# Optimization experiments

Hardware: AMD Instinct MI355X
Metric: run time of the kernel (lower is better)

## Reference

```python
import jax, jax.numpy as jnp
import numpy as np

N = 100000
E = 1600000


def gcn_conv(x, src, dst, W, b, n_nodes):
    # PyG GCNConv: h = x @ W; symmetric norm with self-loops; scatter-add to dst; + bias
    h = x @ W
    deg = jnp.ones((n_nodes,), h.dtype).at[dst].add(jnp.ones((src.shape[0],), h.dtype))  # deg includes self-loop
    dis = jax.lax.rsqrt(deg)  # deg >= 1 so safe
    norm = dis[src] * dis[dst]  # [E]
    agg = jax.ops.segment_sum(norm[:, None] * h[src], dst, num_segments=n_nodes)
    agg = agg + (dis * dis)[:, None] * h  # self-loop contribution (norm = 1/deg_i)
    return agg + b


def setup_inputs() -> dict:
    key = jax.random.key(0)
    ks = jax.random.split(key, 10)
    x = jax.random.normal(ks[0], (N, 500), dtype=jnp.float32)
    edge_index = jax.random.randint(ks[1], (2, E), 0, N, dtype=jnp.int64)
    def glorot(k, fan_in, fan_out):
        s = jnp.sqrt(6.0 / (fan_in + fan_out))
        return jax.random.uniform(k, (fan_in, fan_out), jnp.float32, -s, s)
    return {
        "x": x,
        "edge_index": edge_index,
        "W0": glorot(ks[2], 500, 128), "b0": jnp.zeros((128,), jnp.float32),
        "W1": glorot(ks[3], 128, 128), "b1": jnp.zeros((128,), jnp.float32),
        "W2": glorot(ks[4], 128, 128), "b2": jnp.zeros((128,), jnp.float32),
        "Wfc": glorot(ks[5], 128, 40), "bfc": jnp.zeros((40,), jnp.float32),
    }


def reference(x, edge_index, W0, b0, W1, b1, W2, b2, Wfc, bfc):
    src, dst = edge_index[0], edge_index[1]
    # eval mode: dropout(p=0.2, training=False) is identity
    h = jax.nn.relu(gcn_conv(x, src, dst, W0, b0, N))
    h = jax.nn.relu(gcn_conv(h, src, dst, W1, b1, N))
    h = jax.nn.relu(gcn_conv(h, src, dst, W2, b2, N))
    logits = h @ Wfc + bfc
    return jax.nn.log_softmax(logits, axis=1)
```

## Files before the change

### kernel.cpp

```cpp
#include <hip/hip_runtime.h>
#include <hip/hip_bf16.h>
#include <cstdint>
#include <cstddef>

#define FIN 500
#define FH  128
#define FOUT 40
#define NB 256

typedef __attribute__((ext_vector_type(8))) short short8;
typedef __attribute__((ext_vector_type(4))) float f32x4;

__device__ inline float bf_lo(unsigned v) { unsigned t = v << 16; return __builtin_bit_cast(float, t); }
__device__ inline float bf_hi(unsigned v) { unsigned t = v & 0xffff0000u; return __builtin_bit_cast(float, t); }
__device__ inline unsigned short f2bf_bits(float f) {
  __hip_bfloat16 b = __float2bfloat16(f);
  return __builtin_bit_cast(unsigned short, b);
}


__global__ void __launch_bounds__(256) k_bcount(const int* __restrict__ dst,
                                                int* __restrict__ bucketCnt, int E) {
  __shared__ int lc[NB];
  int t = threadIdx.x;
  lc[t] = 0;
  __syncthreads();
  int base = blockIdx.x * 2048 + t * 8;
#pragma unroll
  for (int j = 0; j < 8; ++j) {
    int e = base + j;
    if (e < E) atomicAdd(&lc[dst[e] >> 9], 1);
  }
  __syncthreads();
  if (lc[t]) atomicAdd(&bucketCnt[t], lc[t]);
}

__global__ void k_bscan(const int* __restrict__ bucketCnt, int* __restrict__ bucketBase) {
  __shared__ int s[NB];
  int t = threadIdx.x;
  int v = bucketCnt[t];
  s[t] = v;
  __syncthreads();
  for (int o = 1; o < NB; o <<= 1) {
    int u = 0;
    if (t >= o) u = s[t - o];
    __syncthreads();
    if (t >= o) s[t] += u;
    __syncthreads();
  }
  bucketBase[t] = s[t] - v;
  if (t == NB - 1) bucketBase[NB] = s[NB - 1];
}

__global__ void __launch_bounds__(256) k_bin(const int* __restrict__ src,
                                             const int* __restrict__ dst,
                                             const int* __restrict__ bucketBase,
                                             int* __restrict__ bucketFill,
                                             int2* __restrict__ ebin, int E) {
  __shared__ int lc[NB];
  __shared__ int lbb[NB];
  int t = threadIdx.x;
  lc[t] = 0;
  lbb[t] = bucketBase[t];
  __syncthreads();
  int base = blockIdx.x * 2048 + t * 8;
  int rk[8], bk[8], dd[8], ss[8];
#pragma unroll
  for (int j = 0; j < 8; ++j) {
    int e = base + j;
    if (e < E) {
      dd[j] = dst[e]; ss[j] = src[e];
      bk[j] = dd[j] >> 9;
      rk[j] = atomicAdd(&lc[bk[j]], 1);
    }
  }
  __syncthreads();
  int c = lc[t];
  int gb = 0;
  if (c) gb = atomicAdd(&bucketFill[t], c);
  __syncthreads();
  lc[t] = gb;
  __syncthreads();
#pragma unroll
  for (int j = 0; j < 8; ++j) {
    int e = base + j;
    if (e < E) {
      int pos = lbb[bk[j]] + lc[bk[j]] + rk[j];
      ebin[pos] = make_int2(ss[j], dd[j]);
    }
  }
}

__global__ void __launch_bounds__(512) k_bhist(const int2* __restrict__ ebin,
                                               const int* __restrict__ bucketBase,
                                               int* __restrict__ cnt, int N) {
  __shared__ int hc[512];
  int t = threadIdx.x, b = blockIdx.x;
  hc[t] = 0;
  __syncthreads();
  int s = bucketBase[b], e = bucketBase[b + 1];
  for (int i = s + t; i < e; i += 512) atomicAdd(&hc[ebin[i].y & 511], 1);
  __syncthreads();
  int idx = b * 512 + t;
  if (idx < N) cnt[idx] = hc[t];
}

__global__ void __launch_bounds__(512) k_fscatter(const int2* __restrict__ ebin,
                                                  const int* __restrict__ bucketBase,
                                                  const int* __restrict__ rp,
                                                  const float* __restrict__ dis,
                                                  int2* __restrict__ epackS, int N) {
  __shared__ int lrp[512];
  __shared__ float ldis[512];
  __shared__ int fill[512];
  int t = threadIdx.x, b = blockIdx.x;
  int n0 = b * 512 + t;
  lrp[t] = (n0 < N) ? rp[n0] : 0;
  ldis[t] = (n0 < N) ? dis[n0] : 0.f;
  fill[t] = 0;
  __syncthreads();
  int s = bucketBase[b], e = bucketBase[b + 1];
  for (int i = s + t; i < e; i += 512) {
    int2 ed = ebin[i];
    int ld = ed.y & 511;
    int r = atomicAdd(&fill[ld], 1);
    float nm = dis[ed.x] * ldis[ld];
    epackS[lrp[ld] + r] = make_int2(ed.x << 7, __builtin_bit_cast(int, nm));
  }
}


__global__ void k_dis(const int* __restrict__ cnt, float* __restrict__ dis, int n) {
  int i = blockIdx.x * 256 + threadIdx.x;
  if (i < n) dis[i] = rsqrtf((float)cnt[i] + 1.0f);
}

__global__ void k_scan1(const int* __restrict__ cnt, int* __restrict__ rp,
                        int* __restrict__ bsums, int n) {
  __shared__ int sums[256];
  int t = threadIdx.x;
  int base = blockIdx.x * 1024;
  int c[4]; int tot = 0;
#pragma unroll
  for (int j = 0; j < 4; ++j) {
    int idx = base + t * 4 + j;
    c[j] = (idx < n) ? cnt[idx] : 0;
    tot += c[j];
  }
  sums[t] = tot;
  __syncthreads();
  for (int off = 1; off < 256; off <<= 1) {
    int v = 0;
    if (t >= off) v = sums[t - off];
    __syncthreads();
    if (t >= off) sums[t] += v;
    __syncthreads();
  }
  int run = sums[t] - tot;
#pragma unroll
  for (int j = 0; j < 4; ++j) {
    int idx = base + t * 4 + j;
    if (idx < n) rp[idx] = run;
    run += c[j];
  }
  if (t == 255) bsums[blockIdx.x] = sums[255];
}

__global__ void k_scan2(int* __restrict__ bsums, int nb) {
  __shared__ int s[256];
  int t = threadIdx.x;
  int v = (t < nb) ? bsums[t] : 0;
  s[t] = v;
  __syncthreads();
  for (int off = 1; off < 256; off <<= 1) {
    int u = 0;
    if (t >= off) u = s[t - off];
    __syncthreads();
    if (t >= off) s[t] += u;
    __syncthreads();
  }
  if (t < nb) bsums[t] = s[t] - v;
}

__global__ void k_scan3(int* __restrict__ rp, const int* __restrict__ bsums, int n, int E) {
  int idx = blockIdx.x * 256 + threadIdx.x;
  if (idx < n) rp[idx] += bsums[idx >> 10];
  if (idx == n) rp[n] = E;
}

__global__ void k_rescale(const int2* __restrict__ epackS, const float* __restrict__ scale,
                          int2* __restrict__ epackL, int E) {
  int e = blockIdx.x * 256 + threadIdx.x;
  if (e >= E) return;
  int2 p = epackS[e];
  float n = __builtin_bit_cast(float, p.y) * scale[p.x >> 7];
  epackL[e] = make_int2(p.x, __builtin_bit_cast(int, n));
}


__global__ void k_prep_w(const float* __restrict__ W, short* __restrict__ WT, int K, int KPAD) {
  int idx = blockIdx.x * 256 + threadIdx.x;
  if (idx >= 128 * KPAD) return;
  int c = idx / KPAD, k = idx - c * KPAD;
  WT[idx] = (k < K) ? (short)f2bf_bits(W[(size_t)k * FH + c]) : (short)0;
}

__global__ void k_prep_wfc(const float* __restrict__ Wfc, short* __restrict__ WfcT) {
  int idx = blockIdx.x * 256 + threadIdx.x;
  if (idx >= 48 * 128) return;
  int c = idx >> 7, k = idx & 127;
  WfcT[idx] = (c < FOUT) ? (short)f2bf_bits(Wfc[(size_t)k * FOUT + c]) : (short)0;
}


template<int KP, bool AF32>
__global__ void __launch_bounds__(512) k_gemm_q(const void* __restrict__ Aptr,
                                                const short* __restrict__ WT,
                                                unsigned char* __restrict__ hQ,
                                                float* __restrict__ scale,
                                                int M, int K) {
  constexpr int KPB = KP * 2;
  constexpr int NKT = KP / 32;
  __shared__ char sB[128 * KPB];
  __shared__ unsigned char lq[8][16 * 128];
  const int tid = threadIdx.x;
  const int wave = tid >> 6, lane = tid & 63;
  const int lr = lane & 15, g = lane >> 4;
  const int swz = (lr & 7) << 4;

  for (int idx = tid; idx < 16 * KP; idx += 512) {
    int c = idx / (KP / 8);
    int kq = idx - c * (KP / 8);
    short8 v = *(const short8*)(WT + (size_t)c * KP + kq * 8);
    *(short8*)(sB + (size_t)c * KPB + ((kq * 16) ^ ((c & 7) << 4))) = v;
  }
  __syncthreads();

  const int nStrips = M >> 4;
  for (int sid = blockIdx.x * 8 + wave; sid < nStrips; sid += gridDim.x * 8) {
    const int rowbase = sid * 16;
    const int arow = rowbase + lr;

    f32x4 acc[8];
#pragma unroll
    for (int j = 0; j < 8; ++j) acc[j] = (f32x4){0.f, 0.f, 0.f, 0.f};

    auto loadA = [&](int kt, short8& dstv) {
      const int k0 = kt * 32 + g * 8;
      if constexpr (AF32) {
        const float* A = (const float*)Aptr + (size_t)arow * K;
        float f[8];
        if (k0 + 8 <= K) {
          float4 u0 = *(const float4*)(A + k0);
          float4 u1 = *(const float4*)(A + k0 + 4);
          f[0] = u0.x; f[1] = u0.y; f[2] = u0.z; f[3] = u0.w;
          f[4] = u1.x; f[5] = u1.y; f[6] = u1.z; f[7] = u1.w;
        } else {
#pragma unroll
          for (int j = 0; j < 8; ++j) f[j] = (k0 + j < K) ? A[k0 + j] : 0.f;
        }
#pragma unroll
        for (int j = 0; j < 8; ++j) dstv[j] = (short)f2bf_bits(f[j]);
      } else {
        dstv = *(const short8*)((const short*)Aptr + (size_t)arow * K + k0);
      }
    };

    short8 aC, aN;
    loadA(0, aC);
#pragma unroll
    for (int kt = 0; kt < NKT; ++kt) {
      if (kt + 1 < NKT) loadA(kt + 1, aN);
      const int kofs = (kt * 64 + g * 16) ^ swz;
#pragma unroll
      for (int j = 0; j < 8; ++j) {
        short8 b = *(const short8*)(sB + (size_t)(j * 16 + lr) * KPB + kofs);
        acc[j] = __builtin_amdgcn_mfma_f32_16x16x32_bf16(aC, b, acc[j], 0, 0, 0);
      }
      aC = aN;
    }

    float mx[4];
#pragma unroll
    for (int r = 0; r < 4; ++r) {
      float m = 0.f;
#pragma unroll
      for (int j = 0; j < 8; ++j) m = fmaxf(m, fabsf(acc[j][r]));
#pragma unroll
      for (int s = 1; s < 16; s <<= 1) m = fmaxf(m, __shfl_xor(m, s));
      mx[r] = m;
    }
    if (lr == 0) {
      float4 sv = make_float4(mx[0] * (1.f / 127.f), mx[1] * (1.f / 127.f),
                              mx[2] * (1.f / 127.f), mx[3] * (1.f / 127.f));
      *(float4*)(scale + rowbase + g * 4) = sv;
    }
    float rs[4];
#pragma unroll
    for (int r = 0; r < 4; ++r) rs[r] = (mx[r] > 0.f) ? 127.f / mx[r] : 0.f;
#pragma unroll
    for (int j = 0; j < 8; ++j) {
#pragma unroll
      for (int r = 0; r < 4; ++r) {
        int q = (int)rintf(acc[j][r] * rs[r]);
        lq[wave][(g * 4 + r) * 128 + j * 16 + lr] = (unsigned char)(signed char)q;
      }
    }
    asm volatile("s_waitcnt lgkmcnt(0)" ::: "memory");
    __builtin_amdgcn_sched_barrier(0);
    {
      int o = lane * 32;
      *(uint4*)(hQ + (size_t)rowbase * 128 + o) = *(const uint4*)(&lq[wave][o]);
      *(uint4*)(hQ + (size_t)rowbase * 128 + o + 16) = *(const uint4*)(&lq[wave][o + 16]);
    }
  }
}


__global__ void __launch_bounds__(256) k_agg(const char* __restrict__ hQbytes,
                                             const float* __restrict__ scale,
                                             char* __restrict__ outbytes,
                                             const float* __restrict__ dis,
                                             const int* __restrict__ rp,
                                             const int2* __restrict__ epackL,
                                             const float* __restrict__ bias,
                                             int N) {
  int node = blockIdx.x * 4 + (threadIdx.x >> 6);
  int lane = threadIdx.x & 63;
  if (node >= N) return;
  const int q = lane & 31;
  const int hi = lane >> 5;
  const int e0 = rp[node], end = rp[node + 1];
  int2 p = make_int2(0, 0);
  if (lane < 16 && e0 + lane < end) p = epackL[e0 + lane];
  float a0 = 0.f, a1 = 0.f, a2 = 0.f, a3 = 0.f;
  if (hi == 0) {
    float w = dis[node]; w = w * w * scale[node];
    int sv = *(const int*)(hQbytes + (size_t)node * 128 + q * 4);
    a0 = w * (float)((sv << 24) >> 24);
    a1 = w * (float)((sv << 16) >> 24);
    a2 = w * (float)((sv << 8) >> 24);
    a3 = w * (float)(sv >> 24);
  }
  const int vbp = hi * 4;
  for (int e = e0; e < end; e += 16) {
    int2 pn = make_int2(0, 0);
    if (lane < 16 && e + 16 + lane < end) pn = epackL[e + 16 + lane];
    int vv[8]; float nn[8];
#pragma unroll
    for (int j = 0; j < 8; ++j) {
      int idx4 = vbp + 8 * j;
      int off = __builtin_amdgcn_ds_bpermute(idx4, p.x);
      int nb  = __builtin_amdgcn_ds_bpermute(idx4, p.y);
      nn[j] = __builtin_bit_cast(float, nb);
      vv[j] = *(const int*)(hQbytes + (size_t)(unsigned)(off + q * 4));
    }
#pragma unroll
    for (int j = 0; j < 8; ++j) {
      int d = vv[j];
      float n = nn[j];
      a0 += n * (float)((d << 24) >> 24);
      a1 += n * (float)((d << 16) >> 24);
      a2 += n * (float)((d << 8) >> 24);
      a3 += n * (float)(d >> 24);
    }
    p = pn;
  }
  a0 += __shfl_xor(a0, 32); a1 += __shfl_xor(a1, 32);
  a2 += __shfl_xor(a2, 32); a3 += __shfl_xor(a3, 32);
  if (hi == 0) {
    float4 bv = *(const float4*)(bias + 4 * q);
    a0 = fmaxf(a0 + bv.x, 0.f); a1 = fmaxf(a1 + bv.y, 0.f);
    a2 = fmaxf(a2 + bv.z, 0.f); a3 = fmaxf(a3 + bv.w, 0.f);
    uint2 r;
    r.x = ((unsigned)f2bf_bits(a1) << 16) | (unsigned)f2bf_bits(a0);
    r.y = ((unsigned)f2bf_bits(a3) << 16) | (unsigned)f2bf_bits(a2);
    *(uint2*)(outbytes + (size_t)node * 256 + q * 8) = r;
  }
}


__global__ void __launch_bounds__(256) k_logits(const short* __restrict__ h,
                                                const short* __restrict__ WfcT,
                                                const float* __restrict__ bfc,
                                                float* __restrict__ out, int N) {
  const int wave = threadIdx.x >> 6, lane = threadIdx.x & 63;
  const int lr = lane & 15, g = lane >> 4;
  const int nbase = blockIdx.x * 64 + wave * 16;
  int arow = nbase + lr; if (arow >= N) arow = N - 1;
  const short* ap = h + (size_t)arow * FH;
  short8 af[4];
#pragma unroll
  for (int ks = 0; ks < 4; ++ks)
    af[ks] = *(const short8*)(ap + ks * 32 + g * 8);
  f32x4 acc[3];
#pragma unroll
  for (int t = 0; t < 3; ++t) {
    acc[t] = (f32x4){0.f, 0.f, 0.f, 0.f};
    const short* bp = WfcT + (size_t)(t * 16 + lr) * FH;
#pragma unroll
    for (int ks = 0; ks < 4; ++ks) {
      short8 bf = *(const short8*)(bp + ks * 32 + g * 8);
      acc[t] = __builtin_amdgcn_mfma_f32_16x16x32_bf16(af[ks], bf, acc[t], 0, 0, 0);
    }
  }
  float bb[3];
#pragma unroll
  for (int t = 0; t < 3; ++t) { int c = t * 16 + lr; bb[t] = (c < FOUT) ? bfc[c] : 0.f; }
  const bool v2 = (lr < 8);
  float res[3][4];
#pragma unroll
  for (int r = 0; r < 4; ++r) {
    float l0 = acc[0][r] + bb[0];
    float l1 = acc[1][r] + bb[1];
    float l2 = v2 ? (acc[2][r] + bb[2]) : -INFINITY;
    float mm = fmaxf(fmaxf(l0, l1), l2);
#pragma unroll
    for (int s = 1; s < 16; s <<= 1) mm = fmaxf(mm, __shfl_xor(mm, s));
    float e0 = expf(l0 - mm), e1 = expf(l1 - mm), e2 = v2 ? expf(l2 - mm) : 0.f;
    float ss = e0 + e1 + e2;
#pragma unroll
    for (int s = 1; s < 16; s <<= 1) ss += __shfl_xor(ss, s);
    float lse = mm + logf(ss);
    res[0][r] = l0 - lse; res[1][r] = l1 - lse; res[2][r] = l2 - lse;
  }
#pragma unroll
  for (int t = 0; t < 3; ++t) {
    int c = t * 16 + lr;
    if (c < FOUT) {
#pragma unroll
      for (int r = 0; r < 4; ++r) {
        int node = nbase + g * 4 + r;
        if (node < N) out[(size_t)node * FOUT + c] = res[t][r];
      }
    }
  }
}


static inline size_t align_up(size_t x, size_t a) { return (x + a - 1) & ~(a - 1); }

extern "C" void kernel_launch(void* const* d_in, const int* in_sizes, int n_in,
                              void* d_out, int out_size, void* d_ws, size_t ws_size,
                              hipStream_t stream) {
  const float* x   = (const float*)d_in[0];
  const int*   ei  = (const int*)d_in[1];
  const float* W0  = (const float*)d_in[2];
  const float* b0  = (const float*)d_in[3];
  const float* W1  = (const float*)d_in[4];
  const float* b1  = (const float*)d_in[5];
  const float* W2  = (const float*)d_in[6];
  const float* b2  = (const float*)d_in[7];
  const float* Wfc = (const float*)d_in[8];
  const float* bfc = (const float*)d_in[9];
  float* out = (float*)d_out;

  const int N = in_sizes[0] / FIN;
  const int E = in_sizes[1] / 2;
  const int* src = ei;
  const int* dst = ei + E;
  const int KP0 = 512;

  char* ws = (char*)d_ws;
  size_t off = 0;
  int* cnt = (int*)(ws + off);            off = align_up(off + (size_t)N * 4, 512);
  float* dis = (float*)(ws + off);        off = align_up(off + (size_t)N * 4, 512);
  int* rp = (int*)(ws + off);             off = align_up(off + (size_t)(N + 1) * 4, 512);
  int* bsums = (int*)(ws + off);          off = align_up(off + 4096, 512);
  int* bucketCnt = (int*)(ws + off);      off = align_up(off + (NB + 1) * 4, 512);
  int* bucketBase = (int*)(ws + off);     off = align_up(off + (NB + 1) * 4, 512);
  int* bucketFill = (int*)(ws + off);     off = align_up(off + (NB + 1) * 4, 512);
  int2* ebin = (int2*)(ws + off);         off = align_up(off + (size_t)E * 8, 512);
  int2* epackS = (int2*)(ws + off);       off = align_up(off + (size_t)E * 8, 512);
  int2* epackL = (int2*)(ws + off);       off = align_up(off + (size_t)E * 8, 512);
  short* WT0 = (short*)(ws + off);        off = align_up(off + (size_t)128 * KP0 * 2, 512);
  short* WT1 = (short*)(ws + off);        off = align_up(off + (size_t)128 * FH * 2, 512);
  short* WT2 = (short*)(ws + off);        off = align_up(off + (size_t)128 * FH * 2, 512);
  short* WfcT = (short*)(ws + off);       off = align_up(off + (size_t)48 * FH * 2, 512);
  short* hB = (short*)(ws + off);         off = align_up(off + (size_t)N * FH * 2, 512);
  float* scale = (float*)(ws + off);      off = align_up(off + (size_t)N * 4, 512);
  unsigned char* hQ = (unsigned char*)ebin;

  const int gE = (E + 255) / 256;
  const int nbScan = (N + 1023) / 1024;
  const int gN4 = (N + 3) / 4;
  const int gBlk = (E + 2047) / 2048;
  const int NBUSE = (N + 511) / 512;

  hipMemsetAsync(bucketCnt, 0, (NB + 1) * 4, stream);
  hipMemsetAsync(bucketFill, 0, (NB + 1) * 4, stream);
  k_bcount<<<gBlk, 256, 0, stream>>>(dst, bucketCnt, E);
  k_bscan<<<1, NB, 0, stream>>>(bucketCnt, bucketBase);
  k_bin<<<gBlk, 256, 0, stream>>>(src, dst, bucketBase, bucketFill, ebin, E);
  k_bhist<<<NBUSE, 512, 0, stream>>>(ebin, bucketBase, cnt, N);
  k_dis<<<(N + 255) / 256, 256, 0, stream>>>(cnt, dis, N);
  k_scan1<<<nbScan, 256, 0, stream>>>(cnt, rp, bsums, N);
  k_scan2<<<1, 256, 0, stream>>>(bsums, nbScan);
  k_scan3<<<(N + 1 + 255) / 256, 256, 0, stream>>>(rp, bsums, N, E);
  k_fscatter<<<NBUSE, 512, 0, stream>>>(ebin, bucketBase, rp, dis, epackS, N);

  k_prep_w<<<(128 * KP0 + 255) / 256, 256, 0, stream>>>(W0, WT0, FIN, KP0);
  k_prep_w<<<(128 * FH + 255) / 256, 256, 0, stream>>>(W1, WT1, FH, FH);
  k_prep_w<<<(128 * FH + 255) / 256, 256, 0, stream>>>(W2, WT2, FH, FH);
  k_prep_wfc<<<(48 * FH + 255) / 256, 256, 0, stream>>>(Wfc, WfcT);

  const int gLog = (N + 63) / 64;

  k_gemm_q<512, true><<<256, 512, 0, stream>>>(x, WT0, hQ, scale, N, FIN);
  k_rescale<<<gE, 256, 0, stream>>>(epackS, scale, epackL, E);
  k_agg<<<gN4, 256, 0, stream>>>((const char*)hQ, scale, (char*)hB, dis, rp, epackL, b0, N);
  k_gemm_q<128, false><<<256, 512, 0, stream>>>(hB, WT1, hQ, scale, N, FH);
  k_rescale<<<gE, 256, 0, stream>>>(epackS, scale, epackL, E);
  k_agg<<<gN4, 256, 0, stream>>>((const char*)hQ, scale, (char*)hB, dis, rp, epackL, b1, N);
  k_gemm_q<128, false><<<256, 512, 0, stream>>>(hB, WT2, hQ, scale, N, FH);
  k_rescale<<<gE, 256, 0, stream>>>(epackS, scale, epackL, E);
  k_agg<<<gN4, 256, 0, stream>>>((const char*)hQ, scale, (char*)hB, dis, rp, epackL, b2, N);
  k_logits<<<gLog, 256, 0, stream>>>(hB, WfcT, bfc, out, N);
}
```

Baseline: 375.3 us.

## Fuse per-edge scale rescale into aggregation, pack binned edges, deepen GEMM A prefetch

The three k_rescale passes are removed. The aggregation kernel now gathers the per-source quantization scale itself and multiplies it into the edge weight before broadcasting it across the wavefront. Binned edges are packed into a single 32-bit word (src<<9 | local dst), which halves the ebin traffic in the binning, histogram and scatter kernels. The GEMM A-operand prefetch now runs two k-steps ahead instead of one. The trade-offs are an extra dependent scale gather inside the aggregation loop, more registers in the GEMM, and a dedicated hQ buffer because it can no longer alias ebin.

```diff
diff --git a/kernel.cpp b/kernel.cpp
--- a/kernel.cpp
+++ b/kernel.cpp
@@ -56,7 +56,7 @@
                                              const int* __restrict__ dst,
                                              const int* __restrict__ bucketBase,
                                              int* __restrict__ bucketFill,
-                                             int2* __restrict__ ebin, int E) {
+                                             unsigned* __restrict__ ebin, int E) {
   __shared__ int lc[NB];
   __shared__ int lbb[NB];
   int t = threadIdx.x;
@@ -64,13 +64,14 @@
   lbb[t] = bucketBase[t];
   __syncthreads();
   int base = blockIdx.x * 2048 + t * 8;
-  int rk[8], bk[8], dd[8], ss[8];
+  int rk[8], bk[8]; unsigned pk[8];
 #pragma unroll
   for (int j = 0; j < 8; ++j) {
     int e = base + j;
     if (e < E) {
-      dd[j] = dst[e]; ss[j] = src[e];
-      bk[j] = dd[j] >> 9;
+      int d = dst[e], s = src[e];
+      bk[j] = d >> 9;
+      pk[j] = ((unsigned)s << 9) | (unsigned)(d & 511);
       rk[j] = atomicAdd(&lc[bk[j]], 1);
     }
   }
@@ -86,12 +87,12 @@
     int e = base + j;
     if (e < E) {
       int pos = lbb[bk[j]] + lc[bk[j]] + rk[j];
-      ebin[pos] = make_int2(ss[j], dd[j]);
-    }
-  }
-}
-
-__global__ void __launch_bounds__(512) k_bhist(const int2* __restrict__ ebin,
+      ebin[pos] = pk[j];
+    }
+  }
+}
+
+__global__ void __launch_bounds__(512) k_bhist(const unsigned* __restrict__ ebin,
                                                const int* __restrict__ bucketBase,
                                                int* __restrict__ cnt, int N) {
   __shared__ int hc[512];
@@ -99,13 +100,13 @@
   hc[t] = 0;
   __syncthreads();
   int s = bucketBase[b], e = bucketBase[b + 1];
-  for (int i = s + t; i < e; i += 512) atomicAdd(&hc[ebin[i].y & 511], 1);
+  for (int i = s + t; i < e; i += 512) atomicAdd(&hc[ebin[i] & 511], 1);
   __syncthreads();
   int idx = b * 512 + t;
   if (idx < N) cnt[idx] = hc[t];
 }
 
-__global__ void __launch_bounds__(512) k_fscatter(const int2* __restrict__ ebin,
+__global__ void __launch_bounds__(512) k_fscatter(const unsigned* __restrict__ ebin,
                                                   const int* __restrict__ bucketBase,
                                                   const int* __restrict__ rp,
                                                   const float* __restrict__ dis,
@@ -121,11 +122,12 @@
   __syncthreads();
   int s = bucketBase[b], e = bucketBase[b + 1];
   for (int i = s + t; i < e; i += 512) {
-    int2 ed = ebin[i];
-    int ld = ed.y & 511;
+    unsigned u = ebin[i];
+    int ld = u & 511;
+    int sn = u >> 9;
     int r = atomicAdd(&fill[ld], 1);
-    float nm = dis[ed.x] * ldis[ld];
-    epackS[lrp[ld] + r] = make_int2(ed.x << 7, __builtin_bit_cast(int, nm));
+    float nm = dis[sn] * ldis[ld];
+    epackS[lrp[ld] + r] = make_int2(sn << 7, __builtin_bit_cast(int, nm));
   }
 }
 
@@ -186,15 +188,6 @@
   int idx = blockIdx.x * 256 + threadIdx.x;
   if (idx < n) rp[idx] += bsums[idx >> 10];
   if (idx == n) rp[n] = E;
-}
-
-__global__ void k_rescale(const int2* __restrict__ epackS, const float* __restrict__ scale,
-                          int2* __restrict__ epackL, int E) {
-  int e = blockIdx.x * 256 + threadIdx.x;
-  if (e >= E) return;
-  int2 p = epackS[e];
-  float n = __builtin_bit_cast(float, p.y) * scale[p.x >> 7];
-  epackL[e] = make_int2(p.x, __builtin_bit_cast(int, n));
 }
 
 
@@ -266,18 +259,19 @@
       }
     };
 
-    short8 aC, aN;
-    loadA(0, aC);
+    short8 aCur, aNx1, aNx2;
+    loadA(0, aCur);
+    if (NKT > 1) loadA(1, aNx1);
 #pragma unroll
     for (int kt = 0; kt < NKT; ++kt) {
-      if (kt + 1 < NKT) loadA(kt + 1, aN);
+      if (kt + 2 < NKT) loadA(kt + 2, aNx2);
       const int kofs = (kt * 64 + g * 16) ^ swz;
 #pragma unroll
       for (int j = 0; j < 8; ++j) {
         short8 b = *(const short8*)(sB + (size_t)(j * 16 + lr) * KPB + kofs);
-        acc[j] = __builtin_amdgcn_mfma_f32_16x16x32_bf16(aC, b, acc[j], 0, 0, 0);
+        acc[j] = __builtin_amdgcn_mfma_f32_16x16x32_bf16(aCur, b, acc[j], 0, 0, 0);
       }
-      aC = aN;
+      aCur = aNx1; aNx1 = aNx2;
     }
 
     float mx[4];
@@ -322,7 +316,7 @@
                                              char* __restrict__ outbytes,
                                              const float* __restrict__ dis,
                                              const int* __restrict__ rp,
-                                             const int2* __restrict__ epackL,
+                                             const int2* __restrict__ epackS,
                                              const float* __restrict__ bias,
                                              int N) {
   int node = blockIdx.x * 4 + (threadIdx.x >> 6);
@@ -332,7 +326,11 @@
   const int hi = lane >> 5;
   const int e0 = rp[node], end = rp[node + 1];
   int2 p = make_int2(0, 0);
-  if (lane < 16 && e0 + lane < end) p = epackL[e0 + lane];
+  float psc = 0.f;
+  if (lane < 16 && e0 + lane < end) {
+    p = epackS[e0 + lane];
+    psc = scale[(unsigned)p.x >> 7];
+  }
   float a0 = 0.f, a1 = 0.f, a2 = 0.f, a3 = 0.f;
   if (hi == 0) {
     float w = dis[node]; w = w * w * scale[node];
@@ -345,13 +343,19 @@
   const int vbp = hi * 4;
   for (int e = e0; e < end; e += 16) {
     int2 pn = make_int2(0, 0);
-    if (lane < 16 && e + 16 + lane < end) pn = epackL[e + 16 + lane];
+    float pnsc = 0.f;
+    if (lane < 16 && e + 16 + lane < end) {
+      pn = epackS[e + 16 + lane];
+      pnsc = scale[(unsigned)pn.x >> 7];
+    }
+    float wcur = __builtin_bit_cast(float, p.y) * psc;
+    int wbits = __builtin_bit_cast(int, wcur);
     int vv[8]; float nn[8];
 #pragma unroll
     for (int j = 0; j < 8; ++j) {
       int idx4 = vbp + 8 * j;
       int off = __builtin_amdgcn_ds_bpermute(idx4, p.x);
-      int nb  = __builtin_amdgcn_ds_bpermute(idx4, p.y);
+      int nb  = __builtin_amdgcn_ds_bpermute(idx4, wbits);
       nn[j] = __builtin_bit_cast(float, nb);
       vv[j] = *(const int*)(hQbytes + (size_t)(unsigned)(off + q * 4));
     }
@@ -364,7 +368,7 @@
       a2 += n * (float)((d << 8) >> 24);
       a3 += n * (float)(d >> 24);
     }
-    p = pn;
+    p = pn; psc = pnsc;
   }
   a0 += __shfl_xor(a0, 32); a1 += __shfl_xor(a1, 32);
   a2 += __shfl_xor(a2, 32); a3 += __shfl_xor(a3, 32);
@@ -470,18 +474,16 @@
   int* bucketCnt = (int*)(ws + off);      off = align_up(off + (NB + 1) * 4, 512);
   int* bucketBase = (int*)(ws + off);     off = align_up(off + (NB + 1) * 4, 512);
   int* bucketFill = (int*)(ws + off);     off = align_up(off + (NB + 1) * 4, 512);
-  int2* ebin = (int2*)(ws + off);         off = align_up(off + (size_t)E * 8, 512);
+  unsigned* ebin = (unsigned*)(ws + off); off = align_up(off + (size_t)E * 4, 512);
   int2* epackS = (int2*)(ws + off);       off = align_up(off + (size_t)E * 8, 512);
-  int2* epackL = (int2*)(ws + off);       off = align_up(off + (size_t)E * 8, 512);
   short* WT0 = (short*)(ws + off);        off = align_up(off + (size_t)128 * KP0 * 2, 512);
   short* WT1 = (short*)(ws + off);        off = align_up(off + (size_t)128 * FH * 2, 512);
   short* WT2 = (short*)(ws + off);        off = align_up(off + (size_t)128 * FH * 2, 512);
   short* WfcT = (short*)(ws + off);       off = align_up(off + (size_t)48 * FH * 2, 512);
   short* hB = (short*)(ws + off);         off = align_up(off + (size_t)N * FH * 2, 512);
   float* scale = (float*)(ws + off);      off = align_up(off + (size_t)N * 4, 512);
-  unsigned char* hQ = (unsigned char*)ebin;
-
-  const int gE = (E + 255) / 256;
+  unsigned char* hQ = (unsigned char*)(ws + off); off = align_up(off + (size_t)N * 128, 512);
+
   const int nbScan = (N + 1023) / 1024;
   const int gN4 = (N + 3) / 4;
   const int gBlk = (E + 2047) / 2048;
@@ -507,13 +509,10 @@
   const int gLog = (N + 63) / 64;
 
   k_gemm_q<512, true><<<256, 512, 0, stream>>>(x, WT0, hQ, scale, N, FIN);
-  k_rescale<<<gE, 256, 0, stream>>>(epackS, scale, epackL, E);
-  k_agg<<<gN4, 256, 0, stream>>>((const char*)hQ, scale, (char*)hB, dis, rp, epackL, b0, N);
+  k_agg<<<gN4, 256, 0, stream>>>((const char*)hQ, scale, (char*)hB, dis, rp, epackS, b0, N);
   k_gemm_q<128, false><<<256, 512, 0, stream>>>(hB, WT1, hQ, scale, N, FH);
-  k_rescale<<<gE, 256, 0, stream>>>(epackS, scale, epackL, E);
-  k_agg<<<gN4, 256, 0, stream>>>((const char*)hQ, scale, (char*)hB, dis, rp, epackL, b1, N);
+  k_agg<<<gN4, 256, 0, stream>>>((const char*)hQ, scale, (char*)hB, dis, rp, epackS, b1, N);
   k_gemm_q<128, false><<<256, 512, 0, stream>>>(hB, WT2, hQ, scale, N, FH);
-  k_rescale<<<gE, 256, 0, stream>>>(epackS, scale, epackL, E);
-  k_agg<<<gN4, 256, 0, stream>>>((const char*)hQ, scale, (char*)hB, dis, rp, epackL, b2, N);
+  k_agg<<<gN4, 256, 0, stream>>>((const char*)hQ, scale, (char*)hB, dis, rp, epackS, b2, N);
   k_logits<<<gLog, 256, 0, stream>>>(hB, WfcT, bfc, out, N);
 }
```

Result: faster. 344.0 us (-8.3%).
